# Kernel tuning notes

Hardware: AMD Instinct MI355X
Metric: run time of the kernel (lower is better)

The kernel has to match this reference:

```python
import jax, jax.numpy as jnp
import numpy as np

B, N, DIM = 2, 4096, 512
HEADS, HEAD_DIM = 8, 64
INNER = HEADS * HEAD_DIM


def setup_inputs() -> dict:
    key = jax.random.key(0)
    k1, k2, k3 = jax.random.split(key, 3)
    x = jax.random.normal(k1, (B, N, DIM), dtype=jnp.float32)
    w_qkv = jax.random.normal(k2, (DIM, 3 * INNER), dtype=jnp.float32) * (DIM ** -0.5)
    temperature = jnp.asarray(np.log(HEAD_DIM ** -0.5), dtype=jnp.float32)
    w_out = jax.random.normal(k3, (INNER, DIM), dtype=jnp.float32) * (INNER ** -0.5)
    b_out = jnp.zeros((DIM,), dtype=jnp.float32)
    return {"x": x, "w_qkv": w_qkv, "temperature": temperature, "w_out": w_out, "b_out": b_out}


def reference(x, w_qkv, temperature, w_out, b_out):
    b, n, _ = x.shape
    qkv = x @ w_qkv                                   # (B, N, 3*inner)
    q, k, v = jnp.split(qkv, 3, axis=-1)
    # Faithful to original: raw reshape (NOT transpose) into (B, H, N, d)
    q = q.reshape(b, HEADS, n, HEAD_DIM)
    k = k.reshape(b, HEADS, n, HEAD_DIM)
    v = v.reshape(b, HEADS, n, HEAD_DIM)
    scores = jnp.einsum('bhnd,bhmd->bhnm', q, k) * jnp.exp(temperature)
    mask = jnp.eye(n, dtype=bool)                     # diagonal self-mask
    mask_value = jnp.finfo(scores.dtype).min
    scores = jnp.where(mask, mask_value, scores)
    attn = jax.nn.softmax(scores, axis=-1)
    out = jnp.einsum('bhnm,bhmd->bhnd', attn, v)      # (B, H, N, d)
    # Faithful to original: raw reshape (NOT transpose) back to (B, N, H*d)
    out = out.reshape(b, n, HEADS * HEAD_DIM)
    return out @ w_out + b_out                        # dropout inactive at inference
```

## Files before the change

### kernel.cpp

```cpp
#include <hip/hip_runtime.h>


typedef __bf16 bf16;
typedef __bf16 bf16x8 __attribute__((ext_vector_type(8)));
typedef __bf16 bf16x4 __attribute__((ext_vector_type(4)));
typedef float  f32x4  __attribute__((ext_vector_type(4)));

#define MFMA_BF16(a, b, c) __builtin_amdgcn_mfma_f32_16x16x32_bf16((a), (b), (c), 0, 0, 0)

__device__ __forceinline__ void gld_lds16(void* lds, const void* g) {
  __builtin_amdgcn_global_load_lds(
      (const __attribute__((address_space(1))) void*)g,
      (__attribute__((address_space(3))) void*)lds, 16, 0, 0);
}


__global__ void cast4_kernel(const float* __restrict__ in, bf16* __restrict__ out, int n4) {
  int i = blockIdx.x * 256 + threadIdx.x;
  if (i >= n4) return;
  float4 v = ((const float4*)in)[i];
  bf16x4 o;
  o[0] = (bf16)v.x; o[1] = (bf16)v.y; o[2] = (bf16)v.z; o[3] = (bf16)v.w;
  *(bf16x4*)(out + 4 * i) = o;
}

__global__ void wtrans_kernel(const float* __restrict__ in, bf16* __restrict__ out, int C) {
  __shared__ float tile[64 * 65];
  const int t = threadIdx.x;
  const int c0 = blockIdx.x * 64, r0 = blockIdx.y * 64;
#pragma unroll
  for (int p = 0; p < 16; p++) {
    int idx = p * 256 + t, r = idx >> 6, c = idx & 63;
    tile[r * 65 + c] = in[(r0 + r) * C + c0 + c];
  }
  __syncthreads();
#pragma unroll
  for (int p = 0; p < 16; p++) {
    int idx = p * 256 + t, c = idx >> 6, r = idx & 63;
    out[(size_t)(c0 + c) * 512 + r0 + r] = (bf16)tile[r * 65 + c];
  }
}

__global__ void vtrans_kernel(const bf16* __restrict__ V, bf16* __restrict__ Vt) {
  __shared__ bf16 tile[64 * 65];
  const int t = threadIdx.x;
  const size_t base = (size_t)blockIdx.y << 18;
  const int n0 = blockIdx.x * 64;
#pragma unroll
  for (int p = 0; p < 16; p++) {
    int idx = p * 256 + t, r = idx >> 6, c = idx & 63;
    tile[r * 65 + c] = V[base + (size_t)(n0 + r) * 64 + c];
  }
  __syncthreads();
#pragma unroll
  for (int p = 0; p < 16; p++) {
    int idx = p * 256 + t, d = idx >> 6, n = idx & 63;
    Vt[base + (size_t)d * 4096 + n0 + n] = tile[n * 65 + d];
  }
}


template<int EPI, int WNT>
__global__ __launch_bounds__(256) void gemm_bt(
    const bf16* __restrict__ A, const bf16* __restrict__ Bt,
    bf16* __restrict__ oQ, bf16* __restrict__ oK, bf16* __restrict__ oV,
    float* __restrict__ oC, const float* __restrict__ bias,
    const float* __restrict__ temp)
{
  __shared__ bf16 As[128 * 32];
  __shared__ bf16 Bs[WNT * 32 * 32];

  const int t    = threadIdx.x;
  const int lane = t & 63;
  const int w    = t >> 6;
  const int mm   = lane & 15;
  const int q    = lane >> 4;
  const int wm   = w >> 1, wn = w & 1;
  const int m0   = blockIdx.y * 128;
  const int n0   = blockIdx.x * (WNT * 32);

  const int srow = t >> 2, sch = t & 3;
  const int gch  = sch ^ ((srow >> 1) & 3);
  const bf16* Ab = A  + (m0 + srow) * 512 + gch * 8;
  const bf16* Bb = Bt + (n0 + srow) * 512 + gch * 8;
  bf16* Asl = As + t * 8;
  bf16* Bsl = Bs + t * 8;

  const int fslot = (q ^ ((mm >> 1) & 3)) * 8;

  const f32x4 zero4 = {0.f, 0.f, 0.f, 0.f};
  f32x4 acc[4][WNT];
#pragma unroll
  for (int i = 0; i < 4; i++)
#pragma unroll
    for (int j = 0; j < WNT; j++) acc[i][j] = zero4;

  for (int k0 = 0; k0 < 512; k0 += 32) {
    __syncthreads();
    gld_lds16(Asl,        Ab + k0);
    gld_lds16(Asl + 2048, Ab + 64 * 512 + k0);
    gld_lds16(Bsl,        Bb + k0);
    if (WNT == 4) gld_lds16(Bsl + 2048, Bb + 64 * 512 + k0);
    __syncthreads();

    bf16x8 af[4], bfv[WNT];
#pragma unroll
    for (int i = 0; i < 4; i++)
      af[i] = *(const bf16x8*)(As + (wm * 64 + i * 16 + mm) * 32 + fslot);
#pragma unroll
    for (int j = 0; j < WNT; j++)
      bfv[j] = *(const bf16x8*)(Bs + (wn * (WNT * 16) + j * 16 + mm) * 32 + fslot);

#pragma unroll
    for (int i = 0; i < 4; i++)
#pragma unroll
      for (int j = 0; j < WNT; j++)
        acc[i][j] = MFMA_BF16(af[i], bfv[j], acc[i][j]);
  }

  if (EPI == 0) {
    const float scale = __expf(temp[0]) * 1.44269504088896f;
#pragma unroll
    for (int i = 0; i < 4; i++) {
      const int row = m0 + wm * 64 + i * 16 + q * 4;
#pragma unroll
      for (int j = 0; j < WNT; j++) {
        const int col = n0 + wn * (WNT * 16) + j * 16 + mm;
        bf16* dst; int c2; float s;
        if (col < 512)       { dst = oQ; c2 = col;        s = scale; }
        else if (col < 1024) { dst = oK; c2 = col - 512;  s = 1.0f;  }
        else                 { dst = oV; c2 = col - 1024; s = 1.0f;  }
#pragma unroll
        for (int r = 0; r < 4; r++)
          dst[(size_t)(row + r) * 512 + c2] = (bf16)(acc[i][j][r] * s);
      }
    }
  } else {
#pragma unroll
    for (int i = 0; i < 4; i++) {
      const int row = m0 + wm * 64 + i * 16 + q * 4;
#pragma unroll
      for (int j = 0; j < WNT; j++) {
        const int col = n0 + wn * (WNT * 16) + j * 16 + mm;
        const float b = bias[col];
#pragma unroll
        for (int r = 0; r < 4; r++)
          oC[(size_t)(row + r) * 512 + col] = acc[i][j][r] + b;
      }
    }
  }
}


template<int SPLIT>
__global__ __launch_bounds__(256, 3) void attn_kernel(
    const bf16* __restrict__ Q, const bf16* __restrict__ Kb,
    const bf16* __restrict__ Vt, bf16* __restrict__ O,
    float* __restrict__ Opart, float* __restrict__ Lpart)
{
  __shared__ bf16 Ks[64 * 64];
  __shared__ bf16 Vs[64 * 64];
  __shared__ bf16 Ps[4 * 64 * 72];

  const int t    = threadIdx.x;
  const int lane = t & 63;
  const int w    = t >> 6;
  const int mm   = lane & 15;
  const int q    = lane >> 4;
  const int bh   = blockIdx.y;
  const int q0   = blockIdx.x * 256;
  const int z    = blockIdx.z;
  const size_t hb = (size_t)bh << 18;
  const bf16* Qh = Q  + hb;
  const bf16* Kh = Kb + hb;
  const bf16* Vh = Vt + hb;
  const int q0w  = q0 + w * 64;

  int tlo, tn;
  if (SPLIT == 1)      { tlo = 0;                               tn = 64; }
  else if (SPLIT == 2) { tlo = z * 32;                          tn = 32; }
  else                 { tlo = (z == 0) ? 0 : (z == 1 ? 22 : 43); tn = (z == 0) ? 22 : 21; }

  bf16x8 qf[4][2];
#pragma unroll
  for (int i = 0; i < 4; i++)
#pragma unroll
    for (int ks = 0; ks < 2; ks++)
      qf[i][ks] = *(const bf16x8*)(Qh + (size_t)(q0w + i * 16 + mm) * 64 + ks * 32 + q * 8);

  const f32x4 zero4 = {0.f, 0.f, 0.f, 0.f};
  f32x4 o[4][4];
  f32x4 lacc[4];
#pragma unroll
  for (int i = 0; i < 4; i++) {
    lacc[i] = zero4;
#pragma unroll
    for (int dj = 0; dj < 4; dj++) o[i][dj] = zero4;
  }

  bf16x8 onesf;
#pragma unroll
  for (int e = 0; e < 8; e++) onesf[e] = (bf16)1.0f;

  const int r0 = t >> 3, c0 = t & 7;
  const int g0 = c0 ^ (r0 & 7);
  bf16* Ksl = Ks + t * 8;
  bf16* Vsl = Vs + t * 8;
  bf16* pw  = Ps + w * (64 * 72);

  for (int it = 0; it < tn; it++) {
    const int kv0 = (tlo + it) * 64;
    __syncthreads();
    gld_lds16(Ksl,        Kh + (size_t)(kv0 + r0) * 64 + g0 * 8);
    gld_lds16(Ksl + 2048, Kh + (size_t)(kv0 + 32 + r0) * 64 + g0 * 8);
    gld_lds16(Vsl,        Vh + (size_t)r0 * 4096 + kv0 + g0 * 8);
    gld_lds16(Vsl + 2048, Vh + (size_t)(32 + r0) * 4096 + kv0 + g0 * 8);
    __syncthreads();

    const bool diag = (kv0 == q0w);

#pragma unroll
    for (int jm = 0; jm < 4; jm++) {
      const int krow = jm * 16 + mm;
      const int sw = krow & 7;
      bf16x8 kf0 = *(const bf16x8*)(Ks + krow * 64 + ((q)     ^ sw) * 8);
      bf16x8 kf1 = *(const bf16x8*)(Ks + krow * 64 + ((4 + q) ^ sw) * 8);
#pragma unroll
      for (int i = 0; i < 4; i++) {
        f32x4 zacc = MFMA_BF16(kf0, qf[i][0], zero4);
        f32x4 sv   = MFMA_BF16(kf1, qf[i][1], zacc);
        if (diag && jm == i && (mm >> 2) == q) sv[mm & 3] = -1e30f;
        bf16x4 pk;
#pragma unroll
        for (int r = 0; r < 4; r++)
          pk[r] = (bf16)__builtin_amdgcn_exp2f(sv[r]);
        *(bf16x4*)(pw + (i * 16 + mm) * 72 + jm * 16 + q * 4) = pk;
      }
    }
    __asm__ volatile("s_waitcnt lgkmcnt(0)" ::: "memory");

#pragma unroll
    for (int ks = 0; ks < 2; ks++) {
      bf16x8 vf[4];
#pragma unroll
      for (int dj = 0; dj < 4; dj++) {
        const int d = dj * 16 + mm;
        vf[dj] = *(const bf16x8*)(Vs + d * 64 + ((ks * 4 + q) ^ (d & 7)) * 8);
      }
#pragma unroll
      for (int i = 0; i < 4; i++) {
        bf16x8 pf = *(const bf16x8*)(pw + (i * 16 + mm) * 72 + ks * 32 + q * 8);
#pragma unroll
        for (int dj = 0; dj < 4; dj++)
          o[i][dj] = MFMA_BF16(pf, vf[dj], o[i][dj]);
        lacc[i] = MFMA_BF16(pf, onesf, lacc[i]);
      }
    }
  }

  if (SPLIT == 1) {
    bf16* Oh = O + hb;
#pragma unroll
    for (int i = 0; i < 4; i++) {
      const int rowb = q0w + i * 16 + q * 4;
#pragma unroll
      for (int r = 0; r < 4; r++) {
        const float rinv = 1.0f / lacc[i][r];
#pragma unroll
        for (int dj = 0; dj < 4; dj++)
          Oh[(size_t)(rowb + r) * 64 + dj * 16 + mm] = (bf16)(o[i][dj][r] * rinv);
      }
    }
  } else {
    float* Op = Opart + ((size_t)z << 22) + hb;
    float* Lp = Lpart + (z << 16) + (bh << 12);
#pragma unroll
    for (int i = 0; i < 4; i++) {
      const int rowb = q0w + i * 16 + q * 4;
      if (mm == 0) {
#pragma unroll
        for (int r = 0; r < 4; r++) Lp[rowb + r] = lacc[i][r];
      }
#pragma unroll
      for (int dj = 0; dj < 4; dj++)
#pragma unroll
        for (int r = 0; r < 4; r++)
          Op[(size_t)(rowb + r) * 64 + dj * 16 + mm] = o[i][dj][r];
    }
  }
}

template<int SPLIT>
__global__ void merge_kernel(const float* __restrict__ Op, const float* __restrict__ Lp,
                             bf16* __restrict__ Ob) {
  const int g = blockIdx.x * 256 + threadIdx.x;
  const int f = g * 4;
  const int row = f >> 6;
  float l = 0.f;
  float4 a = {0.f, 0.f, 0.f, 0.f};
#pragma unroll
  for (int zz = 0; zz < SPLIT; zz++) {
    l += Lp[(zz << 16) + row];
    const float4 b = *(const float4*)(Op + ((size_t)zz << 22) + f);
    a.x += b.x; a.y += b.y; a.z += b.z; a.w += b.w;
  }
  const float rinv = 1.0f / l;
  bf16x4 o;
  o[0] = (bf16)(a.x * rinv);
  o[1] = (bf16)(a.y * rinv);
  o[2] = (bf16)(a.z * rinv);
  o[3] = (bf16)(a.w * rinv);
  *(bf16x4*)(Ob + f) = o;
}


extern "C" void kernel_launch(void* const* d_in, const int* in_sizes, int n_in,
                              void* d_out, int out_size, void* d_ws, size_t ws_size,
                              hipStream_t stream) {
  const float* x      = (const float*)d_in[0];
  const float* w_qkv  = (const float*)d_in[1];
  const float* temp   = (const float*)d_in[2];
  const float* w_out  = (const float*)d_in[3];
  const float* b_out  = (const float*)d_in[4];
  float* out          = (float*)d_out;

  char* ws = (char*)d_ws;
  bf16*  Xb    = (bf16*)(ws);
  bf16*  Wt    = (bf16*)(ws + (size_t)(8u  << 20));
  bf16*  Qb    = (bf16*)(ws + (size_t)(10u << 20));
  bf16*  Kb    = (bf16*)(ws + (size_t)(18u << 20));
  bf16*  Vb    = (bf16*)(ws + (size_t)(26u << 20));
  bf16*  Vtb   = (bf16*)(ws + (size_t)(34u << 20));
  bf16*  Ob    = (bf16*)(ws + (size_t)(42u << 20));
  bf16*  Wot   = (bf16*)(ws + (size_t)(50u << 20));
  float* Lpart = (float*)(ws + (size_t)(51u << 20));
  float* Opart = (float*)(ws + (size_t)(52u << 20));

  const int split = (ws_size >= ((size_t)103u << 20)) ? 3
                  : (ws_size >= ((size_t)86u  << 20)) ? 2 : 1;

  cast4_kernel<<<4096, 256, 0, stream>>>(x, Xb, (8192 * 512) / 4);
  wtrans_kernel<<<dim3(24, 8), 256, 0, stream>>>(w_qkv, Wt, 1536);
  wtrans_kernel<<<dim3(8, 8), 256, 0, stream>>>(w_out, Wot, 512);

  gemm_bt<0, 4><<<dim3(12, 64), 256, 0, stream>>>(Xb, Wt, Qb, Kb, Vb, nullptr, nullptr, temp);

  vtrans_kernel<<<dim3(64, 16), 256, 0, stream>>>(Vb, Vtb);

  if (split == 3) {
    attn_kernel<3><<<dim3(16, 16, 3), 256, 0, stream>>>(Qb, Kb, Vtb, nullptr, Opart, Lpart);
    merge_kernel<3><<<4096, 256, 0, stream>>>(Opart, Lpart, Ob);
  } else if (split == 2) {
    attn_kernel<2><<<dim3(16, 16, 2), 256, 0, stream>>>(Qb, Kb, Vtb, nullptr, Opart, Lpart);
    merge_kernel<2><<<4096, 256, 0, stream>>>(Opart, Lpart, Ob);
  } else {
    attn_kernel<1><<<dim3(16, 16, 1), 256, 0, stream>>>(Qb, Kb, Vtb, Ob, nullptr, nullptr);
  }

  gemm_bt<1, 2><<<dim3(8, 64), 256, 0, stream>>>(Ob, Wot, nullptr, nullptr, nullptr, out, b_out, nullptr);
}
```

Measured before the change: 205.3 us.

## Double-buffer K/V tiles in attention and split P into half-tiles

Adds double-buffered LDS for K and V, so the next tile's global_load_lds is issued before computing the current one and synchronisation uses vmcnt waits and raw barriers. The P scratch is shrunk to a swizzled 32-column half tile, processed in two halves interleaved with the PV MFMAs, and s_setprio raises priority around the MFMA section. The goal is to hide global-load latency and cut LDS footprint. The cost is more LDS for K/V, an extra barrier per iteration, and reliance on hand-placed waitcnt ordering.

```diff
diff --git a/kernel.cpp b/kernel.cpp
--- a/kernel.cpp
+++ b/kernel.cpp
@@ -158,9 +158,9 @@
     const bf16* __restrict__ Vt, bf16* __restrict__ O,
     float* __restrict__ Opart, float* __restrict__ Lpart)
 {
-  __shared__ bf16 Ks[64 * 64];
-  __shared__ bf16 Vs[64 * 64];
-  __shared__ bf16 Ps[4 * 64 * 72];
+  __shared__ bf16 Ks[2][64 * 64];
+  __shared__ bf16 Vs[2][64 * 64];
+  __shared__ bf16 Ps[4][64 * 32];
 
   const int t    = threadIdx.x;
   const int lane = t & 63;
@@ -204,58 +204,83 @@
 
   const int r0 = t >> 3, c0 = t & 7;
   const int g0 = c0 ^ (r0 & 7);
-  bf16* Ksl = Ks + t * 8;
-  bf16* Vsl = Vs + t * 8;
-  bf16* pw  = Ps + w * (64 * 72);
+  const bf16* Kg = Kh + (size_t)r0 * 64 + g0 * 8;
+  const bf16* Vg = Vh + (size_t)r0 * 4096 + g0 * 8;
+  bf16* pw = Ps[w];
+
+  {
+    const int kv0 = tlo * 64;
+    gld_lds16(&Ks[0][t * 8],        Kg + (size_t)kv0 * 64);
+    gld_lds16(&Ks[0][t * 8] + 2048, Kg + (size_t)(kv0 + 32) * 64);
+    gld_lds16(&Vs[0][t * 8],        Vg + kv0);
+    gld_lds16(&Vs[0][t * 8] + 2048, Vg + (size_t)32 * 4096 + kv0);
+  }
 
   for (int it = 0; it < tn; it++) {
+    const int cur = it & 1;
+    if (it + 1 < tn) {
+      const int kv1 = (tlo + it + 1) * 64;
+      bf16* Kn = &Ks[cur ^ 1][t * 8];
+      bf16* Vn = &Vs[cur ^ 1][t * 8];
+      gld_lds16(Kn,        Kg + (size_t)kv1 * 64);
+      gld_lds16(Kn + 2048, Kg + (size_t)(kv1 + 32) * 64);
+      gld_lds16(Vn,        Vg + kv1);
+      gld_lds16(Vn + 2048, Vg + (size_t)32 * 4096 + kv1);
+      __asm__ volatile("s_waitcnt vmcnt(4)" ::: "memory");
+    } else {
+      __asm__ volatile("s_waitcnt vmcnt(0)" ::: "memory");
+    }
+    __builtin_amdgcn_s_barrier();
+    __asm__ volatile("" ::: "memory");
+
     const int kv0 = (tlo + it) * 64;
-    __syncthreads();
-    gld_lds16(Ksl,        Kh + (size_t)(kv0 + r0) * 64 + g0 * 8);
-    gld_lds16(Ksl + 2048, Kh + (size_t)(kv0 + 32 + r0) * 64 + g0 * 8);
-    gld_lds16(Vsl,        Vh + (size_t)r0 * 4096 + kv0 + g0 * 8);
-    gld_lds16(Vsl + 2048, Vh + (size_t)(32 + r0) * 4096 + kv0 + g0 * 8);
-    __syncthreads();
-
     const bool diag = (kv0 == q0w);
-
-#pragma unroll
-    for (int jm = 0; jm < 4; jm++) {
-      const int krow = jm * 16 + mm;
-      const int sw = krow & 7;
-      bf16x8 kf0 = *(const bf16x8*)(Ks + krow * 64 + ((q)     ^ sw) * 8);
-      bf16x8 kf1 = *(const bf16x8*)(Ks + krow * 64 + ((4 + q) ^ sw) * 8);
-#pragma unroll
-      for (int i = 0; i < 4; i++) {
-        f32x4 zacc = MFMA_BF16(kf0, qf[i][0], zero4);
-        f32x4 sv   = MFMA_BF16(kf1, qf[i][1], zacc);
-        if (diag && jm == i && (mm >> 2) == q) sv[mm & 3] = -1e30f;
-        bf16x4 pk;
-#pragma unroll
-        for (int r = 0; r < 4; r++)
-          pk[r] = (bf16)__builtin_amdgcn_exp2f(sv[r]);
-        *(bf16x4*)(pw + (i * 16 + mm) * 72 + jm * 16 + q * 4) = pk;
-      }
-    }
-    __asm__ volatile("s_waitcnt lgkmcnt(0)" ::: "memory");
-
-#pragma unroll
-    for (int ks = 0; ks < 2; ks++) {
+    const bf16* Kc = Ks[cur];
+    const bf16* Vc = Vs[cur];
+
+#pragma unroll
+    for (int h = 0; h < 2; h++) {
+#pragma unroll
+      for (int jj = 0; jj < 2; jj++) {
+        const int jm = 2 * h + jj;
+        const int krow = jm * 16 + mm;
+        const int sw = mm & 7;
+        bf16x8 kf0 = *(const bf16x8*)(Kc + krow * 64 + ((q)     ^ sw) * 8);
+        bf16x8 kf1 = *(const bf16x8*)(Kc + krow * 64 + ((4 + q) ^ sw) * 8);
+#pragma unroll
+        for (int i = 0; i < 4; i++) {
+          f32x4 zacc = MFMA_BF16(kf0, qf[i][0], zero4);
+          f32x4 sv   = MFMA_BF16(kf1, qf[i][1], zacc);
+          if (diag && jm == i && (mm >> 2) == q) sv[mm & 3] = -1e30f;
+          bf16x4 pk;
+#pragma unroll
+          for (int r = 0; r < 4; r++)
+            pk[r] = (bf16)__builtin_amdgcn_exp2f(sv[r]);
+          const int ch = (jj * 2 + (q >> 1)) ^ (mm & 3);
+          *(bf16x4*)(pw + (i * 16 + mm) * 32 + ch * 8 + (q & 1) * 4) = pk;
+        }
+      }
+      __asm__ volatile("s_waitcnt lgkmcnt(0)" ::: "memory");
+
+      __builtin_amdgcn_s_setprio(1);
       bf16x8 vf[4];
 #pragma unroll
       for (int dj = 0; dj < 4; dj++) {
         const int d = dj * 16 + mm;
-        vf[dj] = *(const bf16x8*)(Vs + d * 64 + ((ks * 4 + q) ^ (d & 7)) * 8);
+        vf[dj] = *(const bf16x8*)(Vc + d * 64 + ((h * 4 + q) ^ (d & 7)) * 8);
       }
 #pragma unroll
       for (int i = 0; i < 4; i++) {
-        bf16x8 pf = *(const bf16x8*)(pw + (i * 16 + mm) * 72 + ks * 32 + q * 8);
+        bf16x8 pf = *(const bf16x8*)(pw + (i * 16 + mm) * 32 + (q ^ (mm & 3)) * 8);
 #pragma unroll
         for (int dj = 0; dj < 4; dj++)
           o[i][dj] = MFMA_BF16(pf, vf[dj], o[i][dj]);
         lacc[i] = MFMA_BF16(pf, onesf, lacc[i]);
       }
-    }
+      __builtin_amdgcn_s_setprio(0);
+    }
+    __asm__ volatile("" ::: "memory");
+    __builtin_amdgcn_s_barrier();
   }
 
   if (SPLIT == 1) {
```

Result: no change. 207.4 us (+1.0%).
